# Kernel tuning notes

Measured on AMD Instinct MI355X. Metric: run time of the kernel, lower is better.

The kernel has to match this reference:

```python
import math
import jax, jax.numpy as jnp
import numpy as np

B, T, H, E, K, F = 4, 4096, 512, 8, 2, 2048
CAP_FACTOR, ROUND_TO = 0.3125, 128


def _capacity(num_tokens):
    cap = math.ceil(CAP_FACTOR * num_tokens)
    cap = ROUND_TO * math.ceil(cap / ROUND_TO)
    return max(1, min(cap, num_tokens))


def setup_inputs() -> dict:
    key = jax.random.key(0)
    k0, k1, k2, k3 = jax.random.split(key, 4)
    x = jax.random.normal(k0, (B, T, H), jnp.float32)
    router_w = jax.random.normal(k1, (H, E), jnp.float32) * 0.02
    w1 = jax.random.normal(k2, (E, H, F), jnp.float32) * (1.0 / np.sqrt(H))
    b1 = jnp.zeros((E, F), jnp.float32)
    w2 = jax.random.normal(k3, (E, F, H), jnp.float32) * (1.0 / np.sqrt(F))
    b2 = jnp.zeros((E, H), jnp.float32)
    return {"x": x, "router_w": router_w, "w1": w1, "b1": b1, "w2": w2, "b2": b2}


def reference(x, router_w, w1, b1, w2, b2):
    Bc, Tc, Hc = x.shape
    n = Bc * Tc
    cap = _capacity(n)  # static: 5120
    flat = x.reshape(n, Hc)

    # Router + top-k selection (fp32 logits, softmax over selected logits)
    logits = (flat @ router_w).astype(jnp.float32)          # [n, E]
    sel_logits, expert_idx = jax.lax.top_k(logits, K)       # [n, K]
    weights = jax.nn.softmax(sel_logits, axis=-1)           # [n, K]

    # Flatten (token, k) assignments and sort by expert (stable)
    fe = expert_idx.reshape(-1).astype(jnp.int32)           # [n*K]
    fw = weights.reshape(-1)
    tok = jnp.broadcast_to(jnp.arange(n, dtype=jnp.int32)[:, None], expert_idx.shape).reshape(-1)
    order = jnp.argsort(fe)  # jax sort is stable
    se, st, sw = fe[order], tok[order], fw[order]

    # Per-expert slot index; assignments beyond capacity are dropped
    counts = jnp.bincount(se, length=E)                     # [E]
    offsets = (jnp.cumsum(counts) - counts).astype(jnp.int32)
    slot = jnp.arange(se.shape[0], dtype=jnp.int32) - offsets[se]
    keep = slot < cap
    sw = jnp.where(keep, sw, 0.0)                           # dropped tokens contribute 0

    # Pack into fixed-capacity expert buffers (out-of-range slots dropped)
    sx = flat[st]                                           # [n*K, H]
    expert_inputs = jnp.zeros((E, cap, Hc), flat.dtype).at[se, slot].set(sx, mode='drop')

    # Grouped expert MLP: Dense(F) -> GELU -> Dense(H)
    h = jax.nn.gelu(jnp.einsum('ech,ehf->ecf', expert_inputs, w1) + b1[:, None, :])
    out = jnp.einsum('ecf,efh->ech', h, w2) + b2[:, None, :]

    # Zero invalid (unused) slots
    clipped = jnp.minimum(counts, cap)
    valid = (jnp.arange(cap, dtype=jnp.int32)[None, :] < clipped[:, None])[..., None]
    out = jnp.where(valid, out, 0)

    # Scatter-combine weighted expert outputs back to tokens
    slot_c = jnp.minimum(slot, cap - 1)                     # dropped rows have weight 0
    gathered = out[se, slot_c] * sw[:, None].astype(out.dtype)
    combined = jnp.zeros((n, Hc), out.dtype).at[st].add(gathered)
    return combined.reshape(Bc, Tc, Hc)
```

## Files before the change

### kernel.cpp

```cpp
#include <hip/hip_runtime.h>
#include <hip/hip_bf16.h>

#define NTOK 16384
#define HD   512
#define ED   8
#define FD   2048
#define CAP  5120
#define NA   32768

typedef __bf16 bf16x8 __attribute__((ext_vector_type(8)));
typedef float  f32x4  __attribute__((ext_vector_type(4)));

static constexpr size_t OFF_EIDX = 0;
static constexpr size_t OFF_WGT  = 131072;
static constexpr size_t OFF_STOK = 262144;
static constexpr size_t OFF_ASLOT= 425984;
static constexpr size_t OFF_W2T  = 1u << 20;
static constexpr size_t OFF_H    = OFF_W2T + (size_t)ED*HD*FD*2;
static constexpr size_t OFF_W1T  = OFF_H   + (size_t)ED*CAP*FD*2;
static constexpr size_t OFF_XBF  = OFF_W1T + (size_t)ED*FD*HD*2;
static constexpr size_t OFF_EOUT = OFF_XBF + (size_t)NTOK*HD*2;

__device__ __forceinline__ unsigned short f2bf(float f) {
    __bf16 b = (__bf16)f;
    return __builtin_bit_cast(unsigned short, b);
}
__device__ __forceinline__ unsigned short f2h(float f) {
    _Float16 h = (_Float16)f;
    return __builtin_bit_cast(unsigned short, h);
}
__device__ __forceinline__ float h2f(unsigned short u) {
    return (float)__builtin_bit_cast(_Float16, u);
}

__device__ __forceinline__ float gelu_fast(float v) {
    const float u = 1.5957691216057308f * (v + 0.044715f * v * v * v);
    return v / (1.f + __expf(-u));
}

__device__ __forceinline__ void gl16(const unsigned short* g, unsigned short* l) {
    __builtin_amdgcn_global_load_lds(
        (const __attribute__((address_space(1))) unsigned int*)(const void*)g,
        (__attribute__((address_space(3))) unsigned int*)(void*)l, 16, 0, 0);
}

__global__ __launch_bounds__(256) void transpose_cast_kernel(
    const float* __restrict__ in, unsigned short* __restrict__ out, int R, int C)
{
    __shared__ unsigned short tile[32][33];
    const int e = blockIdx.z;
    in  += (size_t)e * R * C;
    out += (size_t)e * R * C;
    const int r0 = blockIdx.y * 32, c0 = blockIdx.x * 32;
    const int tr = threadIdx.x >> 3, tc = (threadIdx.x & 7) * 4;
    const float4 v = *(const float4*)(in + (size_t)(r0 + tr) * C + c0 + tc);
    tile[tr][tc + 0] = f2bf(v.x);
    tile[tr][tc + 1] = f2bf(v.y);
    tile[tr][tc + 2] = f2bf(v.z);
    tile[tr][tc + 3] = f2bf(v.w);
    __syncthreads();
    ushort4 o;
    o.x = tile[tc + 0][tr]; o.y = tile[tc + 1][tr];
    o.z = tile[tc + 2][tr]; o.w = tile[tc + 3][tr];
    *(ushort4*)(out + (size_t)(c0 + tr) * R + r0 + tc) = o;
}

__global__ __launch_bounds__(256) void router_kernel(
    const float* __restrict__ x, const float* __restrict__ rw,
    int* __restrict__ eidx, float* __restrict__ wgt,
    unsigned short* __restrict__ xbf)
{
    __shared__ float rws[HD * ED];
    const int tid = threadIdx.x;
    for (int i = tid * 4; i < HD * ED; i += 256 * 4)
        *(float4*)(rws + i) = *(const float4*)(rw + i);
    __syncthreads();

    const int wid = tid >> 6, lane = tid & 63;
    const int t = blockIdx.x * 4 + wid;
    const float* xr = x + (size_t)t * HD;

    float acc[ED];
#pragma unroll
    for (int e = 0; e < ED; e++) acc[e] = 0.f;

    float4 xv0 = *(const float4*)(xr + lane * 8);
    float4 xv1 = *(const float4*)(xr + lane * 8 + 4);
    float xv[8] = {xv0.x, xv0.y, xv0.z, xv0.w, xv1.x, xv1.y, xv1.z, xv1.w};

    union { unsigned short us[8]; uint4 v; } pk;
#pragma unroll
    for (int j = 0; j < 8; j++) pk.us[j] = f2bf(xv[j]);
    *(uint4*)(xbf + (size_t)t * HD + lane * 8) = pk.v;

#pragma unroll
    for (int j = 0; j < 8; j++) {
        const int h = lane * 8 + j;
#pragma unroll
        for (int e = 0; e < ED; e++) acc[e] += xv[j] * rws[h * ED + e];
    }
#pragma unroll
    for (int off = 32; off >= 1; off >>= 1) {
#pragma unroll
        for (int e = 0; e < ED; e++) acc[e] += __shfl_down(acc[e], off);
    }
    if (lane == 0) {
        int e0 = 0; float l0 = acc[0];
        for (int e = 1; e < ED; e++) if (acc[e] > l0) { l0 = acc[e]; e0 = e; }
        int e1 = 0; float l1 = -1e30f;
        for (int e = 0; e < ED; e++) {
            if (e == e0) continue;
            if (acc[e] > l1) { l1 = acc[e]; e1 = e; }
        }
        const float ex = expf(l1 - l0);
        const float inv = 1.f / (1.f + ex);
        eidx[t * 2 + 0] = e0;  eidx[t * 2 + 1] = e1;
        wgt [t * 2 + 0] = inv; wgt [t * 2 + 1] = ex * inv;
    }
}

__global__ __launch_bounds__(1024) void scan_kernel(
    const int* __restrict__ eidx,
    int* __restrict__ stok, int* __restrict__ aslot)
{
    __shared__ int running[ED];
    __shared__ int wcnt[16][ED];
    const int tid = threadIdx.x;

    for (int i = tid; i < ED * CAP; i += 1024) stok[i] = -1;
    if (tid < ED) running[tid] = 0;
    __syncthreads();

    const int lane = tid & 63, wid = tid >> 6;
    const unsigned long long below = (1ull << lane) - 1ull;

    for (int c = 0; c < NA / 1024; c++) {
        const int a = c * 1024 + tid;
        const int e = eidx[a];
        int myrank = 0;
#pragma unroll
        for (int ee = 0; ee < ED; ee++) {
            unsigned long long m = __ballot(e == ee);
            if (ee == e) myrank = __popcll(m & below);
            if (lane == 0) wcnt[wid][ee] = __popcll(m);
        }
        __syncthreads();
        int woff = 0;
        for (int ww = 0; ww < wid; ww++) woff += wcnt[ww][e];
        const int slot = running[e] + woff + myrank;
        if (slot < CAP) {
            stok[e * CAP + slot] = a >> 1;
            aslot[a] = slot;
        } else {
            aslot[a] = -1;
        }
        __syncthreads();
        if (tid < ED) {
            int tot = 0;
            for (int ww = 0; ww < 16; ww++) tot += wcnt[ww][tid];
            running[tid] += tot;
        }
        __syncthreads();
    }
}

template<int KD, int ND, int NT, bool G1>
__global__ __launch_bounds__(256) void gemm_mfma(
    const unsigned short* __restrict__ Abase,
    const unsigned short* __restrict__ Bt,
    const float* __restrict__ bias,
    const int* __restrict__ stok,
    unsigned short* __restrict__ hout)
{
    constexpr int BUFE = 128 * 32;
    __shared__ __align__(16) unsigned short As[2 * BUFE];
    __shared__ __align__(16) unsigned short Bs[2 * BUFE];

    const int tid = threadIdx.x;
    const int e  = blockIdx.x & 7;
    const int g  = blockIdx.x >> 3;
    const int n0 = (g % NT) * 128;
    const int m0 = (g / NT) * 128;

    const int lane = tid & 63;
    const int wid  = tid >> 6;

    const int rsub = lane >> 2;
    const int csw  = (lane & 3) ^ ((rsub >> 1) & 3);

    const unsigned short *ag0, *ag1, *bg0, *bg1;
    {
        const int R0 = (wid * 2 + 0) * 16 + rsub;
        const int R1 = (wid * 2 + 1) * 16 + rsub;
        size_t a0, a1;
        if constexpr (G1) {
            const int t0 = stok[e * CAP + m0 + R0];
            const int t1 = stok[e * CAP + m0 + R1];
            a0 = (size_t)(t0 >= 0 ? t0 : 0);
            a1 = (size_t)(t1 >= 0 ? t1 : 0);
        } else {
            a0 = (size_t)(e * CAP + m0 + R0);
            a1 = (size_t)(e * CAP + m0 + R1);
        }
        ag0 = Abase + a0 * KD + csw * 8;
        ag1 = Abase + a1 * KD + csw * 8;
        bg0 = Bt + ((size_t)e * ND + n0 + R0) * KD + csw * 8;
        bg1 = Bt + ((size_t)e * ND + n0 + R1) * KD + csw * 8;
    }
    unsigned short* lA = As + (wid * 2) * 512;
    unsigned short* lB = Bs + (wid * 2) * 512;

    const int wrow = (wid & 1) * 64;
    const int wcol = (wid >> 1) * 64;
    const int l15  = lane & 15;
    const int quad = lane >> 4;
    const int xq   = quad ^ ((l15 >> 1) & 3);
    const int fA   = (wrow + l15) * 32 + xq * 8;
    const int fB   = (wcol + l15) * 32 + xq * 8;

    f32x4 acc[4][4];
#pragma unroll
    for (int i = 0; i < 4; i++)
#pragma unroll
        for (int j = 0; j < 4; j++) acc[i][j] = (f32x4)0.f;

#define STAGE(B, KC)                                                           \
    {                                                                          \
        gl16(ag0 + (KC), lA + (B) * BUFE);                                     \
        gl16(ag1 + (KC), lA + (B) * BUFE + 512);                               \
        gl16(bg0 + (KC), lB + (B) * BUFE);                                     \
        gl16(bg1 + (KC), lB + (B) * BUFE + 512);                               \
    }

#define COMPUTE(B)                                                             \
    {                                                                          \
        const unsigned short* Ab = As + (B) * BUFE;                            \
        const unsigned short* Bb = Bs + (B) * BUFE;                            \
        bf16x8 af[4], bfv[4];                                                  \
        _Pragma("unroll")                                                      \
        for (int i = 0; i < 4; i++) af[i]  = *(const bf16x8*)(Ab + fA + i * 512); \
        _Pragma("unroll")                                                      \
        for (int j = 0; j < 4; j++) bfv[j] = *(const bf16x8*)(Bb + fB + j * 512); \
        _Pragma("unroll")                                                      \
        for (int i = 0; i < 4; i++)                                            \
            _Pragma("unroll")                                                  \
            for (int j = 0; j < 4; j++)                                        \
                acc[i][j] = __builtin_amdgcn_mfma_f32_16x16x32_bf16(           \
                    af[i], bfv[j], acc[i][j], 0, 0, 0);                        \
    }

    STAGE(0, 0);
    __syncthreads();

    for (int kc = 0; kc <= KD - 128; kc += 64) {
        STAGE(1, kc + 32);
        COMPUTE(0);
        __syncthreads();
        STAGE(0, kc + 64);
        COMPUTE(1);
        __syncthreads();
    }
    STAGE(1, KD - 32);
    COMPUTE(0);
    __syncthreads();
    COMPUTE(1);
#undef STAGE
#undef COMPUTE

#pragma unroll
    for (int i = 0; i < 4; i++) {
#pragma unroll
        for (int g2 = 0; g2 < 4; g2++) {
            const int m = wrow + i * 16 + quad * 4 + g2;
            unsigned short* hrow = hout + ((size_t)e * CAP + m0 + m) * ND + n0;
#pragma unroll
            for (int j = 0; j < 4; j++) {
                const int n = wcol + j * 16 + l15;
                const float v = acc[i][j][g2] + bias[(size_t)e * ND + n0 + n];
                hrow[n] = G1 ? f2bf(gelu_fast(v)) : f2h(v);
            }
        }
    }
}

__global__ __launch_bounds__(256) void combine_kernel(
    const unsigned short* __restrict__ eout,
    const int* __restrict__ eidx, const int* __restrict__ aslot,
    const float* __restrict__ wgt, float* __restrict__ out)
{
    const int tid = threadIdx.x;
    const int t  = blockIdx.x * 2 + (tid >> 7);
    const int h0 = (tid & 127) * 4;
    float r0 = 0.f, r1 = 0.f, r2 = 0.f, r3 = 0.f;
#pragma unroll
    for (int k = 0; k < 2; k++) {
        const int a = t * 2 + k;
        const int s = aslot[a];
        if (s >= 0) {
            const float w = wgt[a];
            const int e = eidx[a];
            const ushort4 v = *(const ushort4*)(eout + ((size_t)e * CAP + s) * HD + h0);
            r0 += w * h2f(v.x); r1 += w * h2f(v.y);
            r2 += w * h2f(v.z); r3 += w * h2f(v.w);
        }
    }
    float4 o; o.x = r0; o.y = r1; o.z = r2; o.w = r3;
    *(float4*)(out + (size_t)t * HD + h0) = o;
}

extern "C" void kernel_launch(void* const* d_in, const int* in_sizes, int n_in,
                              void* d_out, int out_size, void* d_ws, size_t ws_size,
                              hipStream_t stream)
{
    const float* x  = (const float*)d_in[0];
    const float* rw = (const float*)d_in[1];
    const float* w1 = (const float*)d_in[2];
    const float* b1 = (const float*)d_in[3];
    const float* w2 = (const float*)d_in[4];
    const float* b2 = (const float*)d_in[5];
    float* out = (float*)d_out;

    char* ws = (char*)d_ws;
    int*   eidx  = (int*)  (ws + OFF_EIDX);
    float* wgt   = (float*)(ws + OFF_WGT);
    int*   stok  = (int*)  (ws + OFF_STOK);
    int*   aslot = (int*)  (ws + OFF_ASLOT);
    unsigned short* w2t  = (unsigned short*)(ws + OFF_W2T);
    unsigned short* hbuf = (unsigned short*)(ws + OFF_H);
    unsigned short* w1t  = (unsigned short*)(ws + OFF_W1T);
    unsigned short* xbf  = (unsigned short*)(ws + OFF_XBF);
    unsigned short* eout = (unsigned short*)(ws + OFF_EOUT);

    transpose_cast_kernel<<<dim3(FD / 32, HD / 32, ED), 256, 0, stream>>>(w1, w1t, HD, FD);
    transpose_cast_kernel<<<dim3(HD / 32, FD / 32, ED), 256, 0, stream>>>(w2, w2t, FD, HD);
    router_kernel<<<NTOK / 4, 256, 0, stream>>>(x, rw, eidx, wgt, xbf);
    scan_kernel<<<1, 1024, 0, stream>>>(eidx, stok, aslot);

    gemm_mfma<HD, FD, FD/128, true>
        <<<8 * (FD/128) * (CAP/128), 256, 0, stream>>>(
        xbf, w1t, b1, stok, hbuf);

    gemm_mfma<FD, HD, HD/128, false>
        <<<8 * (HD/128) * (CAP/128), 256, 0, stream>>>(
        hbuf, w2t, b2, nullptr, eout);

    combine_kernel<<<NTOK / 2, 256, 0, stream>>>(eout, eidx, aslot, wgt, out);
}
```

Measured before the change: 526.5 us.

## Skip empty expert tiles, swap MFMA operands for vectorized epilogue, cheaper GELU

The scan kernel now writes per-expert clipped counts, and both GEMMs exit early for 128-row tiles beyond an expert's used capacity, avoiding MFMA work on padding rows. The MFMA operands are swapped so each lane holds four consecutive output columns, letting the epilogue load bias as float4 and store four bf16/fp16 values at once instead of scalar stores. GELU is rewritten with an FMA-based polynomial and a hardware reciprocal. Skipped rows of the intermediate buffers are left unwritten; this relies on combine only reading valid slots, and the rcp approximation slightly changes numerics.

New measurement: 464.6 us. -11.8%, faster.

```diff
diff --git a/kernel.cpp b/kernel.cpp
--- a/kernel.cpp
+++ b/kernel.cpp
@@ -15,6 +15,7 @@
 static constexpr size_t OFF_WGT  = 131072;
 static constexpr size_t OFF_STOK = 262144;
 static constexpr size_t OFF_ASLOT= 425984;
+static constexpr size_t OFF_ECNT = 557056;
 static constexpr size_t OFF_W2T  = 1u << 20;
 static constexpr size_t OFF_H    = OFF_W2T + (size_t)ED*HD*FD*2;
 static constexpr size_t OFF_W1T  = OFF_H   + (size_t)ED*CAP*FD*2;
@@ -34,8 +35,10 @@
 }
 
 __device__ __forceinline__ float gelu_fast(float v) {
-    const float u = 1.5957691216057308f * (v + 0.044715f * v * v * v);
-    return v / (1.f + __expf(-u));
+    const float t = v * v;
+    const float u = v * fmaf(t, 0.0713548214f, 1.5957691216f);
+    const float e = __expf(-u);
+    return v * __builtin_amdgcn_rcpf(1.f + e);
 }
 
 __device__ __forceinline__ void gl16(const unsigned short* g, unsigned short* l) {
@@ -121,7 +124,7 @@
 
 __global__ __launch_bounds__(1024) void scan_kernel(
     const int* __restrict__ eidx,
-    int* __restrict__ stok, int* __restrict__ aslot)
+    int* __restrict__ stok, int* __restrict__ aslot, int* __restrict__ ecnt)
 {
     __shared__ int running[ED];
     __shared__ int wcnt[16][ED];
@@ -162,6 +165,7 @@
         }
         __syncthreads();
     }
+    if (tid < ED) ecnt[tid] = running[tid] < CAP ? running[tid] : CAP;
 }
 
 template<int KD, int ND, int NT, bool G1>
@@ -170,6 +174,7 @@
     const unsigned short* __restrict__ Bt,
     const float* __restrict__ bias,
     const int* __restrict__ stok,
+    const int* __restrict__ ecnt,
     unsigned short* __restrict__ hout)
 {
     constexpr int BUFE = 128 * 32;
@@ -181,6 +186,8 @@
     const int g  = blockIdx.x >> 3;
     const int n0 = (g % NT) * 128;
     const int m0 = (g / NT) * 128;
+
+    if (m0 >= ecnt[e]) return;
 
     const int lane = tid & 63;
     const int wid  = tid >> 6;
@@ -246,7 +253,7 @@
             _Pragma("unroll")                                                  \
             for (int j = 0; j < 4; j++)                                        \
                 acc[i][j] = __builtin_amdgcn_mfma_f32_16x16x32_bf16(           \
-                    af[i], bfv[j], acc[i][j], 0, 0, 0);                        \
+                    bfv[j], af[i], acc[i][j], 0, 0, 0);                        \
     }
 
     STAGE(0, 0);
@@ -269,16 +276,25 @@
 
 #pragma unroll
     for (int i = 0; i < 4; i++) {
-#pragma unroll
-        for (int g2 = 0; g2 < 4; g2++) {
-            const int m = wrow + i * 16 + quad * 4 + g2;
-            unsigned short* hrow = hout + ((size_t)e * CAP + m0 + m) * ND + n0;
-#pragma unroll
-            for (int j = 0; j < 4; j++) {
-                const int n = wcol + j * 16 + l15;
-                const float v = acc[i][j][g2] + bias[(size_t)e * ND + n0 + n];
-                hrow[n] = G1 ? f2bf(gelu_fast(v)) : f2h(v);
+        unsigned short* hrow = hout
+            + ((size_t)e * CAP + m0 + wrow + i * 16 + l15) * ND
+            + n0 + wcol + quad * 4;
+#pragma unroll
+        for (int j = 0; j < 4; j++) {
+            const float4 b4 = *(const float4*)(
+                bias + (size_t)e * ND + n0 + wcol + j * 16 + quad * 4);
+            const float v0 = acc[i][j][0] + b4.x;
+            const float v1 = acc[i][j][1] + b4.y;
+            const float v2 = acc[i][j][2] + b4.z;
+            const float v3 = acc[i][j][3] + b4.w;
+            ushort4 o;
+            if constexpr (G1) {
+                o.x = f2bf(gelu_fast(v0)); o.y = f2bf(gelu_fast(v1));
+                o.z = f2bf(gelu_fast(v2)); o.w = f2bf(gelu_fast(v3));
+            } else {
+                o.x = f2h(v0); o.y = f2h(v1); o.z = f2h(v2); o.w = f2h(v3);
             }
+            *(ushort4*)(hrow + j * 16) = o;
         }
     }
 }
@@ -325,6 +341,7 @@
     float* wgt   = (float*)(ws + OFF_WGT);
     int*   stok  = (int*)  (ws + OFF_STOK);
     int*   aslot = (int*)  (ws + OFF_ASLOT);
+    int*   ecnt  = (int*)  (ws + OFF_ECNT);
     unsigned short* w2t  = (unsigned short*)(ws + OFF_W2T);
     unsigned short* hbuf = (unsigned short*)(ws + OFF_H);
     unsigned short* w1t  = (unsigned short*)(ws + OFF_W1T);
@@ -334,15 +351,15 @@
     transpose_cast_kernel<<<dim3(FD / 32, HD / 32, ED), 256, 0, stream>>>(w1, w1t, HD, FD);
     transpose_cast_kernel<<<dim3(HD / 32, FD / 32, ED), 256, 0, stream>>>(w2, w2t, FD, HD);
     router_kernel<<<NTOK / 4, 256, 0, stream>>>(x, rw, eidx, wgt, xbf);
-    scan_kernel<<<1, 1024, 0, stream>>>(eidx, stok, aslot);
+    scan_kernel<<<1, 1024, 0, stream>>>(eidx, stok, aslot, ecnt);
 
     gemm_mfma<HD, FD, FD/128, true>
         <<<8 * (FD/128) * (CAP/128), 256, 0, stream>>>(
-        xbf, w1t, b1, stok, hbuf);
+        xbf, w1t, b1, stok, ecnt, hbuf);
 
     gemm_mfma<FD, HD, HD/128, false>
         <<<8 * (HD/128) * (CAP/128), 256, 0, stream>>>(
-        hbuf, w2t, b2, nullptr, eout);
+        hbuf, w2t, b2, nullptr, ecnt, eout);
 
     combine_kernel<<<NTOK / 2, 256, 0, stream>>>(eout, eidx, aslot, wgt, out);
 }
```
